# Kernel optimization log

Measured on AMD Instinct MI355X. Metric: run time of the kernel, lower is better.

Reference implementation:

```python
import jax, jax.numpy as jnp
import numpy as np

B, S, E = 8, 2048, 128
DECAY = 1.2
LN_EPS = 1e-3  # keras LayerNormalization default epsilon


def setup_inputs() -> dict:
    key = jax.random.key(0)
    k1, k2, k3, k4 = jax.random.split(key, 4)
    return {
        "x": jax.random.normal(k1, (B, S, E), dtype=jnp.float32),
        "dense_w": jax.random.normal(k2, (E, E), dtype=jnp.float32) * 0.02,
        "dense_b": jnp.zeros((E,), dtype=jnp.float32),
        "concept_map": jax.random.normal(k3, (E, E, E), dtype=jnp.float32) * 0.02,
        "ln_gamma": jnp.ones((E,), dtype=jnp.float32),
        "ln_beta": jnp.zeros((E,), dtype=jnp.float32),
    }


def reference(x, dense_w, dense_b, concept_map, ln_gamma, ln_beta):
    # Dense projection
    h = x @ dense_w + dense_b  # (B, S, E)
    b, s, e = h.shape

    # Decayed prefix-sum recurrence: s_i = (s_{i-1} + h_{i-1}) / 1.2, s_0 = 0
    def step(carry, xt):
        new = (carry + xt) / DECAY
        return new, new

    h_t = jnp.swapaxes(h, 0, 1)  # (S, B, E)
    _, s_tail = jax.lax.scan(step, jnp.zeros((b, e), h.dtype), h_t[:-1])
    s_seq = jnp.concatenate([jnp.zeros((1, b, e), h.dtype), s_tail], axis=0)
    s_seq = jnp.swapaxes(s_seq, 0, 1)  # (B, S, E)

    # result[b,s,c] = sum_{a,p} h[b,s,a] * s_seq[b,s,p] * W[c,a,p]
    # (original code materializes (B,S,E,E,E); this is the fused contraction)
    out = jnp.einsum("bsa,bsp,cap->bsc", h, s_seq, concept_map)

    r = out + h
    # LayerNormalization over the last axis
    mean = jnp.mean(r, axis=-1, keepdims=True)
    var = jnp.var(r, axis=-1, keepdims=True)
    r = (r - mean) * jax.lax.rsqrt(var + LN_EPS) * ln_gamma + ln_beta
    # Dropout is identity at inference
    return r
```

## Files before the change

kernel.cpp:

```cpp
#include <hip/hip_runtime.h>
#include <hip/hip_bf16.h>
#include <math.h>

#define E_DIM 128
#define S_LEN 2048
#define B_N   8
#define BS    (B_N * S_LEN)
#define CHUNK 64
#define NCHUNK (S_LEN / CHUNK)

typedef unsigned short u16;
typedef _Float16 f16;
typedef _Float16 f16x2 __attribute__((ext_vector_type(2)));
typedef _Float16 f16x8 __attribute__((ext_vector_type(8)));
typedef float    f32x16 __attribute__((ext_vector_type(16)));

__global__ __launch_bounds__(256) void k_dense(const float* __restrict__ x,
                                               const float* __restrict__ w,
                                               const float* __restrict__ bias,
                                               float* __restrict__ hout) {
    __shared__ float Wl[E_DIM * E_DIM];
    const int t = threadIdx.x;
    const long r0 = (long)blockIdx.x * 64;

    float4* Wl4 = (float4*)Wl;
    const float4* w4 = (const float4*)w;
#pragma unroll
    for (int i = 0; i < 16; ++i) Wl4[t + 256 * i] = w4[t + 256 * i];
    __syncthreads();

    const int cq = t & 31;
    const int rg = t >> 5;
    float4 bb = ((const float4*)bias)[cq];
    float acc[8][4];
#pragma unroll
    for (int i = 0; i < 8; ++i) {
        acc[i][0] = bb.x; acc[i][1] = bb.y; acc[i][2] = bb.z; acc[i][3] = bb.w;
    }
#pragma unroll 4
    for (int k = 0; k < E_DIM; ++k) {
        float4 wv = Wl4[k * 32 + cq];
#pragma unroll
        for (int i = 0; i < 8; ++i) {
            float xv = x[(r0 + rg * 8 + i) * E_DIM + k];
            acc[i][0] += xv * wv.x;
            acc[i][1] += xv * wv.y;
            acc[i][2] += xv * wv.z;
            acc[i][3] += xv * wv.w;
        }
    }
    float4* h4 = (float4*)(hout + r0 * E_DIM);
#pragma unroll
    for (int i = 0; i < 8; ++i) {
        float4 o;
        o.x = acc[i][0]; o.y = acc[i][1]; o.z = acc[i][2]; o.w = acc[i][3];
        h4[(rg * 8 + i) * 32 + cq] = o;
    }
}

__global__ __launch_bounds__(128) void k_scan(const float* __restrict__ h,
                                              u16* __restrict__ sb16,
                                              float* __restrict__ fc,
                                              u16* __restrict__ hT) {
    const int b = blockIdx.x >> 5;
    const int j = blockIdx.x & 31;
    const int e = threadIdx.x;
    const float inv_d = (float)(1.0 / 1.2);
    const int pos0 = b * S_LEN + j * CHUNK;
    long base = (long)pos0 * E_DIM + e;
    float carry = 0.f;
    union { u16 u[8]; uint4 v; } hb;
#pragma unroll 1
    for (int i0 = 0; i0 < CHUNK; i0 += 8) {
#pragma unroll
        for (int k = 0; k < 8; ++k) {
            float hv = h[base + (long)(i0 + k) * E_DIM];
            union { f16 f; u16 u; } cu; cu.f = (f16)carry;
            sb16[base + (long)(i0 + k) * E_DIM] = cu.u;
            union { f16 f; u16 u; } hu; hu.f = (f16)hv;
            hb.u[k] = hu.u;
            carry = (carry + hv) * inv_d;
        }
        *(uint4*)&hT[(size_t)e * BS + pos0 + i0] = hb.v;
    }
    fc[(b * NCHUNK + j) * E_DIM + e] = carry;
}

__global__ __launch_bounds__(256) void k_carry(float* __restrict__ fc, float dm64) {
    int t = blockIdx.x * 256 + threadIdx.x;
    int b = t >> 7, e = t & 127;
    float c = 0.f;
    for (int j = 0; j < NCHUNK; ++j) {
        int idx = (b * NCHUNK + j) * E_DIM + e;
        float v = fc[idx];
        fc[idx] = c;
        c = v + c * dm64;
    }
}

__global__ __launch_bounds__(256) void k_fix(u16* __restrict__ sb16,
                                             const float* __restrict__ fc) {
    const float L2D = 0.26303440583379383f;
    int u = blockIdx.x * 256 + threadIdx.x;
    int e8  = u & 15;
    int pos = u >> 4;
    int i = pos & (CHUNK - 1);
    int j = (pos >> 6) & (NCHUNK - 1);
    int b = pos >> 11;
    float f = exp2f(-L2D * (float)i);
    const float4* fp = (const float4*)(fc + ((size_t)(b * NCHUNK + j)) * E_DIM + e8 * 8);
    float4 c0 = fp[0], c1 = fp[1];
    float cs[8] = {c0.x, c0.y, c0.z, c0.w, c1.x, c1.y, c1.z, c1.w};
    uint4* sp = (uint4*)(sb16 + (size_t)pos * E_DIM + e8 * 8);
    union { uint4 v; u16 u[8]; } su; su.v = *sp;
#pragma unroll
    for (int k = 0; k < 8; ++k) {
        union { f16 f; u16 u; } a; a.u = su.u[k];
        union { f16 f; u16 u; } o; o.f = (f16)((float)a.f + cs[k] * f);
        su.u[k] = o.u;
    }
    *sp = su.v;
}

__global__ __launch_bounds__(256) void k_wconv(const float* __restrict__ cm,
                                               u16* __restrict__ wb) {
    int t = blockIdx.x * 256 + threadIdx.x;
    int qs = t & 15, c = (t >> 4) & 127, a = t >> 11;
    const float* src = cm + (((long)(c << 7) + a) << 7) + ((qs ^ (c & 15)) << 3);
    float4 v0 = ((const float4*)src)[0];
    float4 v1 = ((const float4*)src)[1];
    union { f16 f[8]; uint4 v; } o;
    o.f[0] = (f16)v0.x; o.f[1] = (f16)v0.y; o.f[2] = (f16)v0.z; o.f[3] = (f16)v0.w;
    o.f[4] = (f16)v1.x; o.f[5] = (f16)v1.y; o.f[6] = (f16)v1.z; o.f[7] = (f16)v1.w;
    ((uint4*)wb)[t] = o.v;
}

__global__ __launch_bounds__(512, 2) void k_main(const u16* __restrict__ hT,
                                                 const u16* __restrict__ sb16,
                                                 const u16* __restrict__ wb,
                                                 float* __restrict__ out) {
    __shared__ u16 Wl[2][16384];
    const int t = threadIdx.x;
    const int w = t >> 6, l = t & 63;
    const int l31 = l & 31, hi = l >> 5;
    const int mb = blockIdx.x >> 2, r = blockIdx.x & 3;
    const int rbp = w >> 1, ntp = w & 1;
    const int row0 = mb * 256 + rbp * 64 + l31;

    f16x2 s2[2][32];
#pragma unroll
    for (int rb = 0; rb < 2; ++rb) {
        const uint4* sp = (const uint4*)(sb16 + (size_t)(row0 + 32 * rb) * E_DIM + hi * 8);
#pragma unroll
        for (int ks = 0; ks < 8; ++ks) {
            union { uint4 u; f16x2 h2[4]; } uu;
            uu.u = sp[ks * 2];
#pragma unroll
            for (int q = 0; q < 4; ++q) s2[rb][ks * 4 + q] = uu.h2[q];
        }
    }

    f32x16 acc[2][2];
#pragma unroll
    for (int rb = 0; rb < 2; ++rb)
#pragma unroll
        for (int nt = 0; nt < 2; ++nt)
#pragma unroll
            for (int g = 0; g < 16; ++g) acc[rb][nt][g] = 0.f;

    const u16* wbK = wb + (size_t)(r * 32) * 16384;
    const u16* hTb = hT + (size_t)(r * 32) * BS + mb * 256 + rbp * 64 + l31;

#define STAGE(buf, sl) {                                                          \
    const u16* gsrc = wbK + (size_t)(sl) * 16384 + t * 8;                         \
    _Pragma("unroll")                                                             \
    for (int i = 0; i < 4; ++i)                                                   \
        __builtin_amdgcn_global_load_lds(                                         \
            (const __attribute__((address_space(1))) void*)(gsrc + i * 4096),     \
            (__attribute__((address_space(3))) void*)&Wl[buf][t * 8 + i * 4096],  \
            16, 0, 0); }

    STAGE(0, 0);
    u16 h0 = hTb[0], h1 = hTb[32];
    __syncthreads();

    const int sxb = l31 & 15;
    const int wcbase = (ntp * 64 + l31) * E_DIM;

#pragma unroll 1
    for (int sl = 0; sl < 32; ++sl) {
        const int cur = sl & 1;
        if (sl < 31) {
            if (cur) STAGE(0, sl + 1) else STAGE(1, sl + 1);
        }
        u16 nh0 = 0, nh1 = 0;
        if (sl < 31) { nh0 = hTb[(size_t)(sl + 1) * BS]; nh1 = hTb[(size_t)(sl + 1) * BS + 32]; }

        union { u16 u[2]; f16x2 v; } hu0, hu1;
        hu0.u[0] = h0; hu0.u[1] = h0;
        hu1.u[0] = h1; hu1.u[1] = h1;
        const u16* Wc = &Wl[cur][wcbase];
#pragma unroll
        for (int ks = 0; ks < 8; ++ks) {
            const int sx = ((ks << 1) + hi) ^ sxb;
            f16x8 b0 = *(const f16x8*)(Wc + sx * 8);
            f16x8 b1 = *(const f16x8*)(Wc + 32 * E_DIM + sx * 8);
            union { f16x2 h2[4]; f16x8 v; } a0, a1;
#pragma unroll
            for (int q = 0; q < 4; ++q) {
                a0.h2[q] = hu0.v * s2[0][ks * 4 + q];
                a1.h2[q] = hu1.v * s2[1][ks * 4 + q];
            }
            acc[0][0] = __builtin_amdgcn_mfma_f32_32x32x16_f16(a0.v, b0, acc[0][0], 0, 0, 0);
            acc[0][1] = __builtin_amdgcn_mfma_f32_32x32x16_f16(a0.v, b1, acc[0][1], 0, 0, 0);
            acc[1][0] = __builtin_amdgcn_mfma_f32_32x32x16_f16(a1.v, b0, acc[1][0], 0, 0, 0);
            acc[1][1] = __builtin_amdgcn_mfma_f32_32x32x16_f16(a1.v, b1, acc[1][1], 0, 0, 0);
        }
        h0 = nh0; h1 = nh1;
        __syncthreads();
    }
#undef STAGE

#pragma unroll
    for (int rb = 0; rb < 2; ++rb)
#pragma unroll
        for (int nt = 0; nt < 2; ++nt)
#pragma unroll
            for (int g = 0; g < 16; ++g) {
                int rowl = (g & 3) + 8 * (g >> 2) + 4 * hi;
                long row = (long)mb * 256 + rbp * 64 + rb * 32 + rowl;
                int col = ntp * 64 + nt * 32 + l31;
                unsafeAtomicAdd(&out[row * E_DIM + col], acc[rb][nt][g]);
            }
}

__global__ __launch_bounds__(256) void k_ln(float* __restrict__ out,
                                            const float* __restrict__ h,
                                            const float* __restrict__ gamma,
                                            const float* __restrict__ beta) {
    const int t = threadIdx.x;
    const int l32 = t & 31, rl = t >> 5;
    const long row = (long)blockIdx.x * 8 + rl;
    float4 v  = ((const float4*)out)[row * 32 + l32];
    float4 hv = ((const float4*)h)[row * 32 + l32];
    v.x += hv.x; v.y += hv.y; v.z += hv.z; v.w += hv.w;
    float ls = v.x + v.y + v.z + v.w;
    float lq = v.x * v.x + v.y * v.y + v.z * v.z + v.w * v.w;
#pragma unroll
    for (int m = 1; m < 32; m <<= 1) {
        ls += __shfl_xor(ls, m, 64);
        lq += __shfl_xor(lq, m, 64);
    }
    float mean = ls * (1.f / 128.f);
    float var  = lq * (1.f / 128.f) - mean * mean;
    float inv  = rsqrtf(var + 1e-3f);
    float4 g = ((const float4*)gamma)[l32];
    float4 b = ((const float4*)beta)[l32];
    float4 o;
    o.x = (v.x - mean) * inv * g.x + b.x;
    o.y = (v.y - mean) * inv * g.y + b.y;
    o.z = (v.z - mean) * inv * g.z + b.z;
    o.w = (v.w - mean) * inv * g.w + b.w;
    ((float4*)out)[row * 32 + l32] = o;
}

extern "C" void kernel_launch(void* const* d_in, const int* in_sizes, int n_in,
                              void* d_out, int out_size, void* d_ws, size_t ws_size,
                              hipStream_t stream) {
    const float* x     = (const float*)d_in[0];
    const float* dw    = (const float*)d_in[1];
    const float* db    = (const float*)d_in[2];
    const float* cm    = (const float*)d_in[3];
    const float* gamma = (const float*)d_in[4];
    const float* beta  = (const float*)d_in[5];
    float* outp = (float*)d_out;

    float* ws = (float*)d_ws;
    float* h   = ws;
    float* fc  = ws + (size_t)BS * E_DIM;
    u16*   wb  = (u16*)(fc + B_N * NCHUNK * E_DIM);
    u16*   hT  = wb + (size_t)E_DIM * E_DIM * E_DIM / 2;
    hT = wb + (size_t)2097152;
    u16*   sb16 = hT + (size_t)BS * E_DIM;

    float dm64 = (float)pow(1.2, -64.0);

    hipMemsetAsync(d_out, 0, (size_t)BS * E_DIM * sizeof(float), stream);
    k_wconv<<<dim3(1024), dim3(256), 0, stream>>>(cm, wb);
    k_dense<<<dim3(BS / 64), dim3(256), 0, stream>>>(x, dw, db, h);
    k_scan <<<dim3(B_N * NCHUNK), dim3(128), 0, stream>>>(h, sb16, fc, hT);
    k_carry<<<dim3(4), dim3(256), 0, stream>>>(fc, dm64);
    k_fix  <<<dim3((BS * E_DIM / 8) / 256), dim3(256), 0, stream>>>(sb16, fc);
    k_main <<<dim3(256), dim3(512), 0, stream>>>(hT, sb16, wb, outp);
    k_ln   <<<dim3(BS / 8), dim3(256), 0, stream>>>(outp, h, gamma, beta);
}
```

Measured before the change: 128.0 us.

## Fuse carry propagation and fix into main kernel, merge weight conversion with dense

Removes the separate k_carry and k_fix launches. Each k_main block now recomputes its chunk carry prefix from the per-chunk final carries and applies the decayed correction while loading s into registers. k_wconv and k_dense are merged into a single launch, and k_main is reshaped to 256-thread blocks over 128 rows with twice as many blocks. This cuts launch overhead and one read-modify-write pass over sb16, at the cost of redundant serial carry loops in every block.

```diff
diff --git a/kernel.cpp b/kernel.cpp
--- a/kernel.cpp
+++ b/kernel.cpp
@@ -15,23 +15,37 @@
 typedef _Float16 f16x8 __attribute__((ext_vector_type(8)));
 typedef float    f32x16 __attribute__((ext_vector_type(16)));
 
-__global__ __launch_bounds__(256) void k_dense(const float* __restrict__ x,
-                                               const float* __restrict__ w,
-                                               const float* __restrict__ bias,
-                                               float* __restrict__ hout) {
+__global__ __launch_bounds__(256) void k_pre(const float* __restrict__ x,
+                                             const float* __restrict__ dw,
+                                             const float* __restrict__ db,
+                                             const float* __restrict__ cm,
+                                             float* __restrict__ hout,
+                                             u16* __restrict__ wb) {
+    if (blockIdx.x < 1024) {
+        int t = blockIdx.x * 256 + threadIdx.x;
+        int qs = t & 15, c = (t >> 4) & 127, a = t >> 11;
+        const float* src = cm + (((long)(c << 7) + a) << 7) + ((qs ^ (c & 15)) << 3);
+        float4 v0 = ((const float4*)src)[0];
+        float4 v1 = ((const float4*)src)[1];
+        union { f16 f[8]; uint4 v; } o;
+        o.f[0] = (f16)v0.x; o.f[1] = (f16)v0.y; o.f[2] = (f16)v0.z; o.f[3] = (f16)v0.w;
+        o.f[4] = (f16)v1.x; o.f[5] = (f16)v1.y; o.f[6] = (f16)v1.z; o.f[7] = (f16)v1.w;
+        ((uint4*)wb)[t] = o.v;
+        return;
+    }
     __shared__ float Wl[E_DIM * E_DIM];
     const int t = threadIdx.x;
-    const long r0 = (long)blockIdx.x * 64;
+    const long r0 = (long)(blockIdx.x - 1024) * 64;
 
     float4* Wl4 = (float4*)Wl;
-    const float4* w4 = (const float4*)w;
+    const float4* w4 = (const float4*)dw;
 #pragma unroll
     for (int i = 0; i < 16; ++i) Wl4[t + 256 * i] = w4[t + 256 * i];
     __syncthreads();
 
     const int cq = t & 31;
     const int rg = t >> 5;
-    float4 bb = ((const float4*)bias)[cq];
+    float4 bb = ((const float4*)db)[cq];
     float acc[8][4];
 #pragma unroll
     for (int i = 0; i < 8; ++i) {
@@ -86,106 +100,84 @@
     fc[(b * NCHUNK + j) * E_DIM + e] = carry;
 }
 
-__global__ __launch_bounds__(256) void k_carry(float* __restrict__ fc, float dm64) {
-    int t = blockIdx.x * 256 + threadIdx.x;
-    int b = t >> 7, e = t & 127;
-    float c = 0.f;
-    for (int j = 0; j < NCHUNK; ++j) {
-        int idx = (b * NCHUNK + j) * E_DIM + e;
-        float v = fc[idx];
-        fc[idx] = c;
-        c = v + c * dm64;
-    }
-}
-
-__global__ __launch_bounds__(256) void k_fix(u16* __restrict__ sb16,
-                                             const float* __restrict__ fc) {
-    const float L2D = 0.26303440583379383f;
-    int u = blockIdx.x * 256 + threadIdx.x;
-    int e8  = u & 15;
-    int pos = u >> 4;
-    int i = pos & (CHUNK - 1);
-    int j = (pos >> 6) & (NCHUNK - 1);
-    int b = pos >> 11;
-    float f = exp2f(-L2D * (float)i);
-    const float4* fp = (const float4*)(fc + ((size_t)(b * NCHUNK + j)) * E_DIM + e8 * 8);
-    float4 c0 = fp[0], c1 = fp[1];
-    float cs[8] = {c0.x, c0.y, c0.z, c0.w, c1.x, c1.y, c1.z, c1.w};
-    uint4* sp = (uint4*)(sb16 + (size_t)pos * E_DIM + e8 * 8);
-    union { uint4 v; u16 u[8]; } su; su.v = *sp;
-#pragma unroll
-    for (int k = 0; k < 8; ++k) {
-        union { f16 f; u16 u; } a; a.u = su.u[k];
-        union { f16 f; u16 u; } o; o.f = (f16)((float)a.f + cs[k] * f);
-        su.u[k] = o.u;
-    }
-    *sp = su.v;
-}
-
-__global__ __launch_bounds__(256) void k_wconv(const float* __restrict__ cm,
-                                               u16* __restrict__ wb) {
-    int t = blockIdx.x * 256 + threadIdx.x;
-    int qs = t & 15, c = (t >> 4) & 127, a = t >> 11;
-    const float* src = cm + (((long)(c << 7) + a) << 7) + ((qs ^ (c & 15)) << 3);
-    float4 v0 = ((const float4*)src)[0];
-    float4 v1 = ((const float4*)src)[1];
-    union { f16 f[8]; uint4 v; } o;
-    o.f[0] = (f16)v0.x; o.f[1] = (f16)v0.y; o.f[2] = (f16)v0.z; o.f[3] = (f16)v0.w;
-    o.f[4] = (f16)v1.x; o.f[5] = (f16)v1.y; o.f[6] = (f16)v1.z; o.f[7] = (f16)v1.w;
-    ((uint4*)wb)[t] = o.v;
-}
-
-__global__ __launch_bounds__(512, 2) void k_main(const u16* __restrict__ hT,
+__global__ __launch_bounds__(256, 2) void k_main(const u16* __restrict__ hT,
                                                  const u16* __restrict__ sb16,
+                                                 const float* __restrict__ fc,
                                                  const u16* __restrict__ wb,
-                                                 float* __restrict__ out) {
+                                                 float* __restrict__ out,
+                                                 float dm64) {
     __shared__ u16 Wl[2][16384];
+    __shared__ float carr[2][E_DIM];
     const int t = threadIdx.x;
     const int w = t >> 6, l = t & 63;
     const int l31 = l & 31, hi = l >> 5;
     const int mb = blockIdx.x >> 2, r = blockIdx.x & 3;
     const int rbp = w >> 1, ntp = w & 1;
-    const int row0 = mb * 256 + rbp * 64 + l31;
-
-    f16x2 s2[2][32];
-#pragma unroll
-    for (int rb = 0; rb < 2; ++rb) {
-        const uint4* sp = (const uint4*)(sb16 + (size_t)(row0 + 32 * rb) * E_DIM + hi * 8);
-#pragma unroll
-        for (int ks = 0; ks < 8; ++ks) {
-            union { uint4 u; f16x2 h2[4]; } uu;
-            uu.u = sp[ks * 2];
-#pragma unroll
-            for (int q = 0; q < 4; ++q) s2[rb][ks * 4 + q] = uu.h2[q];
-        }
-    }
-
-    f32x16 acc[2][2];
-#pragma unroll
-    for (int rb = 0; rb < 2; ++rb)
-#pragma unroll
-        for (int nt = 0; nt < 2; ++nt)
-#pragma unroll
-            for (int g = 0; g < 16; ++g) acc[rb][nt][g] = 0.f;
 
     const u16* wbK = wb + (size_t)(r * 32) * 16384;
-    const u16* hTb = hT + (size_t)(r * 32) * BS + mb * 256 + rbp * 64 + l31;
 
 #define STAGE(buf, sl) {                                                          \
     const u16* gsrc = wbK + (size_t)(sl) * 16384 + t * 8;                         \
     _Pragma("unroll")                                                             \
-    for (int i = 0; i < 4; ++i)                                                   \
+    for (int i = 0; i < 8; ++i)                                                   \
         __builtin_amdgcn_global_load_lds(                                         \
-            (const __attribute__((address_space(1))) void*)(gsrc + i * 4096),     \
-            (__attribute__((address_space(3))) void*)&Wl[buf][t * 8 + i * 4096],  \
+            (const __attribute__((address_space(1))) void*)(gsrc + i * 2048),     \
+            (__attribute__((address_space(3))) void*)&Wl[buf][t * 8 + i * 2048],  \
             16, 0, 0); }
 
     STAGE(0, 0);
-    u16 h0 = hTb[0], h1 = hTb[32];
+
+    const int row_base = mb * 128;
+    const int bb = row_base >> 11;
+    const int j0 = (row_base >> 6) & 31;
+    {
+        const int ch = t >> 7;
+        const int e  = t & 127;
+        const int jend = j0 + ch;
+        float c = 0.f;
+        for (int jj = 0; jj < jend; ++jj)
+            c = fc[(bb * NCHUNK + jj) * E_DIM + e] + c * dm64;
+        carr[ch][e] = c;
+    }
     __syncthreads();
 
+    const float L2D = 0.26303440583379383f;
+    f16x2 s2[2][32];
+#pragma unroll
+    for (int rb = 0; rb < 2; ++rb) {
+        const int row = row_base + rbp * 64 + rb * 32 + l31;
+        const float f = exp2f(-L2D * (float)(row & 63));
+        const uint4* sp = (const uint4*)(sb16 + (size_t)row * E_DIM + hi * 8);
+#pragma unroll
+        for (int ks = 0; ks < 8; ++ks) {
+            union { uint4 u; u16 us[8]; } uu; uu.u = sp[ks * 2];
+            const float* cp = &carr[rbp][ks * 16 + hi * 8];
+#pragma unroll
+            for (int q = 0; q < 4; ++q) {
+                union { f16 f; u16 u; } a0; a0.u = uu.us[2 * q];
+                union { f16 f; u16 u; } a1; a1.u = uu.us[2 * q + 1];
+                f16x2 pr;
+                pr.x = (f16)((float)a0.f + cp[2 * q] * f);
+                pr.y = (f16)((float)a1.f + cp[2 * q + 1] * f);
+                s2[rb][ks * 4 + q] = pr;
+            }
+        }
+    }
+
+    f32x16 acc[2][2];
+#pragma unroll
+    for (int rb = 0; rb < 2; ++rb)
+#pragma unroll
+        for (int nt = 0; nt < 2; ++nt)
+#pragma unroll
+            for (int g = 0; g < 16; ++g) acc[rb][nt][g] = 0.f;
+
+    const u16* hTb = hT + (size_t)mb * 128 + rbp * 64 + l31;
+    u16 h0 = hTb[(size_t)(r * 32) * BS];
+    u16 h1 = hTb[(size_t)(r * 32) * BS + 32];
+
     const int sxb = l31 & 15;
-    const int wcbase = (ntp * 64 + l31) * E_DIM;
+    const int wcoff = (ntp * 64 + l31) * E_DIM;
 
 #pragma unroll 1
     for (int sl = 0; sl < 32; ++sl) {
@@ -194,12 +186,15 @@
             if (cur) STAGE(0, sl + 1) else STAGE(1, sl + 1);
         }
         u16 nh0 = 0, nh1 = 0;
-        if (sl < 31) { nh0 = hTb[(size_t)(sl + 1) * BS]; nh1 = hTb[(size_t)(sl + 1) * BS + 32]; }
+        if (sl < 31) {
+            nh0 = hTb[(size_t)(r * 32 + sl + 1) * BS];
+            nh1 = hTb[(size_t)(r * 32 + sl + 1) * BS + 32];
+        }
 
         union { u16 u[2]; f16x2 v; } hu0, hu1;
         hu0.u[0] = h0; hu0.u[1] = h0;
         hu1.u[0] = h1; hu1.u[1] = h1;
-        const u16* Wc = &Wl[cur][wcbase];
+        const u16* Wc = &Wl[cur][wcoff];
 #pragma unroll
         for (int ks = 0; ks < 8; ++ks) {
             const int sx = ((ks << 1) + hi) ^ sxb;
@@ -228,7 +223,7 @@
 #pragma unroll
             for (int g = 0; g < 16; ++g) {
                 int rowl = (g & 3) + 8 * (g >> 2) + 4 * hi;
-                long row = (long)mb * 256 + rbp * 64 + rb * 32 + rowl;
+                long row = (long)row_base + rbp * 64 + rb * 32 + rowl;
                 int col = ntp * 64 + nt * 32 + l31;
                 unsafeAtomicAdd(&out[row * E_DIM + col], acc[rb][nt][g]);
             }
@@ -276,21 +271,17 @@
     float* outp = (float*)d_out;
 
     float* ws = (float*)d_ws;
-    float* h   = ws;
-    float* fc  = ws + (size_t)BS * E_DIM;
-    u16*   wb  = (u16*)(fc + B_N * NCHUNK * E_DIM);
-    u16*   hT  = wb + (size_t)E_DIM * E_DIM * E_DIM / 2;
-    hT = wb + (size_t)2097152;
+    float* h    = ws;
+    float* fc   = ws + (size_t)BS * E_DIM;
+    u16*   wb   = (u16*)(fc + B_N * NCHUNK * E_DIM);
+    u16*   hT   = wb + (size_t)2097152;
     u16*   sb16 = hT + (size_t)BS * E_DIM;
 
     float dm64 = (float)pow(1.2, -64.0);
 
     hipMemsetAsync(d_out, 0, (size_t)BS * E_DIM * sizeof(float), stream);
-    k_wconv<<<dim3(1024), dim3(256), 0, stream>>>(cm, wb);
-    k_dense<<<dim3(BS / 64), dim3(256), 0, stream>>>(x, dw, db, h);
-    k_scan <<<dim3(B_N * NCHUNK), dim3(128), 0, stream>>>(h, sb16, fc, hT);
-    k_carry<<<dim3(4), dim3(256), 0, stream>>>(fc, dm64);
-    k_fix  <<<dim3((BS * E_DIM / 8) / 256), dim3(256), 0, stream>>>(sb16, fc);
-    k_main <<<dim3(256), dim3(512), 0, stream>>>(hT, sb16, wb, outp);
-    k_ln   <<<dim3(BS / 8), dim3(256), 0, stream>>>(outp, h, gamma, beta);
-}
+    k_pre <<<dim3(1280), dim3(256), 0, stream>>>(x, dw, db, cm, h, wb);
+    k_scan<<<dim3(B_N * NCHUNK), dim3(128), 0, stream>>>(h, sb16, fc, hT);
+    k_main<<<dim3(512), dim3(256), 0, stream>>>(hT, sb16, fc, wb, outp, dm64);
+    k_ln  <<<dim3(BS / 8), dim3(256), 0, stream>>>(outp, h, gamma, beta);
+}
```

Result: no change. 129.7 us (+1.4%).
